# Optimization experiments

Hardware: AMD Instinct MI355X
Metric: run time of the kernel (lower is better)

## Reference

```python
import jax, jax.numpy as jnp
import numpy as np

D_MODEL = 1024
NUM_HEADS = 16
D_K = D_MODEL // NUM_HEADS
THETA = 10000.0
MAX_SEQ_LEN = 2048


def _rope_tables(token_positions):
    # theta^(-2i/d_k) for i in [0, d_k/2)
    inv_freq = THETA ** (-jnp.arange(0, D_K, 2, dtype=jnp.float32) / D_K)
    m_theta = token_positions.astype(jnp.float32)[:, None] * inv_freq[None, :]  # (S, d_k/2)
    return jnp.cos(m_theta), jnp.sin(m_theta)


def _apply_rope(x, cos, sin):
    # x: (B, H, S, d_k); interleaved even/odd pairing
    x1 = x[..., 0::2]
    x2 = x[..., 1::2]
    c = cos[None, None, :, :]
    s = sin[None, None, :, :]
    r1 = x1 * c - x2 * s
    r2 = x1 * s + x2 * c
    return jnp.stack((r1, r2), axis=-1).reshape(x.shape)


def setup_inputs() -> dict:
    key = jax.random.key(0)
    k_x, k_q, k_k, k_v, k_o = jax.random.split(key, 5)
    B, S = 2, 2048
    std = 0.02
    return {
        "x": jax.random.normal(k_x, (B, S, D_MODEL), dtype=jnp.float32),
        "wq": jax.random.normal(k_q, (D_MODEL, D_MODEL), dtype=jnp.float32) * std,
        "wk": jax.random.normal(k_k, (D_MODEL, D_MODEL), dtype=jnp.float32) * std,
        "wv": jax.random.normal(k_v, (D_MODEL, D_MODEL), dtype=jnp.float32) * std,
        "wo": jax.random.normal(k_o, (D_MODEL, D_MODEL), dtype=jnp.float32) * std,
        "token_positions": jnp.arange(S, dtype=jnp.int32),
    }


def reference(x, wq, wk, wv, wo, token_positions):
    B, S, _ = x.shape
    cos, sin = _rope_tables(token_positions)

    # Projections: weight stored as (out, in), applied as x @ W^T
    q = (x @ wq.T).reshape(B, S, NUM_HEADS, D_K).transpose(0, 2, 1, 3)
    k = (x @ wk.T).reshape(B, S, NUM_HEADS, D_K).transpose(0, 2, 1, 3)
    v = (x @ wv.T).reshape(B, S, NUM_HEADS, D_K).transpose(0, 2, 1, 3)

    q = _apply_rope(q, cos, sin)
    k = _apply_rope(k, cos, sin)

    scale = 1.0 / jnp.sqrt(jnp.float32(D_K))
    scores = jnp.einsum("bhqd,bhkd->bhqk", q, k) * scale  # (B, H, S, S)
    causal = jnp.tril(jnp.ones((S, S), dtype=bool))
    scores = jnp.where(causal[None, None, :, :], scores, jnp.finfo(scores.dtype).min)
    probs = jax.nn.softmax(scores, axis=-1)

    out = jnp.einsum("bhqk,bhkd->bhqd", probs, v)  # (B, H, S, d_k)
    out = out.transpose(0, 2, 1, 3).reshape(B, S, D_MODEL)
    return out @ wo.T
```

## Files before the change

kernel.cpp:

```cpp
#include <hip/hip_runtime.h>
#include <hip/hip_bf16.h>
#include <stdint.h>

typedef __attribute__((ext_vector_type(4))) float f32x4;
typedef __attribute__((ext_vector_type(16))) float f32x16;
typedef __bf16 bf16x8v __attribute__((ext_vector_type(8)));
typedef __attribute__((ext_vector_type(4))) unsigned int u32x4;
typedef __attribute__((ext_vector_type(2))) unsigned int u32x2;

constexpr int NB = 2;
constexpr int NS = 2048;
constexpr int ND = 1024;
constexpr int NH = 16;
constexpr int NDK = 64;

__device__ __forceinline__ void gload16(const void* g, void* l) {
    __builtin_amdgcn_global_load_lds(
        (const __attribute__((address_space(1))) unsigned int*)g,
        (__attribute__((address_space(3))) unsigned int*)l, 16, 0, 0);
}

__device__ __forceinline__ unsigned pack_bf16x2(float lo, float hi) {
    unsigned short a = __builtin_bit_cast(unsigned short, (__bf16)lo);
    unsigned short b = __builtin_bit_cast(unsigned short, (__bf16)hi);
    return (unsigned)a | ((unsigned)b << 16);
}

__device__ __forceinline__ float xhalf(float v, int h) {
    const unsigned u = __builtin_bit_cast(unsigned, v);
    const u32x2 r = __builtin_amdgcn_permlane32_swap(u, u, false, false);
    return __builtin_bit_cast(float, h ? r[0] : r[1]);
}

__global__ void __launch_bounds__(256)
prep_kernel(const float* __restrict__ x, const float* __restrict__ wq,
            const float* __restrict__ wk, const float* __restrict__ wv,
            const float* __restrict__ wo, const int* __restrict__ pos,
            __bf16* __restrict__ xb, __bf16* __restrict__ wqb,
            __bf16* __restrict__ wkb, __bf16* __restrict__ wvb,
            __bf16* __restrict__ wob,
            float* __restrict__ cos_t, float* __restrict__ sin_t)
{
    int b = blockIdx.x;
    if (b >= 4096) {
        const int idx = (b - 4096) * 256 + threadIdx.x;
        const int s = idx >> 5, p = idx & 31;
        const float freq = __expf((float)p * (-0.28782313662425572f));
        const float ang = (float)pos[s] * freq;
        float sn, cs;
        sincosf(ang, &sn, &cs);
        cos_t[idx] = cs;
        sin_t[idx] = sn;
        return;
    }
    const float* s; __bf16* d;
    if (b < 2048)      { s = x;  d = xb;            }
    else if (b < 2560) { s = wq; d = wqb; b -= 2048; }
    else if (b < 3072) { s = wk; d = wkb; b -= 2560; }
    else if (b < 3584) { s = wv; d = wvb; b -= 3072; }
    else               { s = wo; d = wob; b -= 3584; }
    const size_t i = ((size_t)b * 256 + threadIdx.x) * 8;
    const f32x4 v0 = *(const f32x4*)(s + i);
    const f32x4 v1 = *(const f32x4*)(s + i + 4);
    bf16x8v o;
#pragma unroll
    for (int j = 0; j < 4; ++j) { o[j] = (__bf16)v0[j]; o[4+j] = (__bf16)v1[j]; }
    *(bf16x8v*)(d + i) = o;
}

__device__ __forceinline__ void epi_one(
    f32x4 a, int fm, int fn, int bm, int wm, int g, int c, int mode, int h_out,
    const float* __restrict__ cos_t, const float* __restrict__ sin_t,
    __bf16* __restrict__ qw, __bf16* __restrict__ kw, __bf16* __restrict__ vtw)
{
    const int m0 = bm * 128 + wm * 64 + fm * 16 + g * 4;
    const int bI = m0 >> 11, s0 = m0 & (NS - 1);
    const int d = fn * 16 + c;
    float v0 = a[0], v1 = a[1], v2 = a[2], v3 = a[3];
    if (mode < 2) {
        const int p = d >> 1;
        const bool odd = (d & 1);
        const float sc = (mode == 0) ? 0.18033688011112042f : 1.0f;
#define ROPE1(V, I)                                                        \
        {                                                                  \
            const float cs = cos_t[(s0 + (I)) * 32 + p];                   \
            const float sn = sin_t[(s0 + (I)) * 32 + p];                   \
            const float oth = __shfl_xor(V, 1, 64);                       \
            V = (odd ? (oth * sn + V * cs) : (V * cs - oth * sn)) * sc;    \
        }
        ROPE1(v0, 0) ROPE1(v1, 1) ROPE1(v2, 2) ROPE1(v3, 3)
#undef ROPE1
        __bf16* dq = (mode == 0) ? qw : kw;
        __bf16* b = dq + (((size_t)bI * NH + h_out) * NS + s0) * NDK + d;
        b[0] = (__bf16)v0; b[NDK] = (__bf16)v1;
        b[2 * NDK] = (__bf16)v2; b[3 * NDK] = (__bf16)v3;
    } else {
        ushort4 pk;
        pk.x = __builtin_bit_cast(unsigned short, (__bf16)v0);
        pk.y = __builtin_bit_cast(unsigned short, (__bf16)v1);
        pk.z = __builtin_bit_cast(unsigned short, (__bf16)v2);
        pk.w = __builtin_bit_cast(unsigned short, (__bf16)v3);
        *(ushort4*)&vtw[(((size_t)bI * NH + h_out) * NDK + d) * NS + s0] = pk;
    }
}

__global__ void __launch_bounds__(256, 3)
qkv_kernel(const __bf16* __restrict__ xb,
           const __bf16* __restrict__ wqb, const __bf16* __restrict__ wkb,
           const __bf16* __restrict__ wvb,
           const float* __restrict__ cos_t, const float* __restrict__ sin_t,
           __bf16* __restrict__ qw, __bf16* __restrict__ kw,
           __bf16* __restrict__ vtw)
{
    __shared__ __align__(16) __bf16 a_lds[128 * 64];
    __shared__ __align__(16) __bf16 b_lds[128 * 64];

    const int t = threadIdx.x, w = t >> 6, lane = t & 63;
    const int g = lane >> 4, c = lane & 15;
    const int bm = blockIdx.x, bn = blockIdx.y;
    const int mode = bn >> 3, nblk = bn & 7;
    const __bf16* wsel = (mode == 0) ? wqb : (mode == 1) ? wkb : wvb;
    const int wm = w >> 1, wn = w & 1;

    f32x4 acc00 = {}, acc01 = {}, acc02 = {}, acc03 = {};
    f32x4 acc10 = {}, acc11 = {}, acc12 = {}, acc13 = {};
    f32x4 acc20 = {}, acc21 = {}, acc22 = {}, acc23 = {};
    f32x4 acc30 = {}, acc31 = {}, acc32 = {}, acc33 = {};

    const int csw = ((t & 7) ^ ((t >> 3) & 7)) * 8;
    const int sx = c & 7;
    const int sl0 = (g ^ sx) * 8;
    const int sl1 = ((4 + g) ^ sx) * 8;
    const __bf16* arow = &a_lds[(wm * 64 + c) * 64];
    const __bf16* brow = &b_lds[(wn * 64 + c) * 64];

    for (int kt = 0; kt < 16; ++kt) {
        __syncthreads();
#pragma unroll
        for (int j = 0; j < 4; ++j) {
            const int r = (j * 256 + t) >> 3;
            gload16(xb   + (size_t)(bm   * 128 + r) * ND + kt * 64 + csw,
                    &a_lds[j * 2048 + w * 512]);
            gload16(wsel + (size_t)(nblk * 128 + r) * ND + kt * 64 + csw,
                    &b_lds[j * 2048 + w * 512]);
        }
        __syncthreads();
#define MM(FM, FN, AF, BF) acc##FM##FN = __builtin_amdgcn_mfma_f32_16x16x32_bf16( \
        AF, BF, acc##FM##FN, 0, 0, 0);
#define KKSTEP(SL)                                                            \
        {                                                                     \
            const bf16x8v af0 = *(const bf16x8v*)(arow + (SL));               \
            const bf16x8v af1 = *(const bf16x8v*)(arow + 1024 + (SL));        \
            const bf16x8v af2 = *(const bf16x8v*)(arow + 2048 + (SL));        \
            const bf16x8v af3 = *(const bf16x8v*)(arow + 3072 + (SL));        \
            const bf16x8v bf0 = *(const bf16x8v*)(brow + (SL));               \
            const bf16x8v bf1 = *(const bf16x8v*)(brow + 1024 + (SL));        \
            const bf16x8v bf2 = *(const bf16x8v*)(brow + 2048 + (SL));        \
            const bf16x8v bf3 = *(const bf16x8v*)(brow + 3072 + (SL));        \
            MM(0,0,af0,bf0) MM(0,1,af0,bf1) MM(0,2,af0,bf2) MM(0,3,af0,bf3)   \
            MM(1,0,af1,bf0) MM(1,1,af1,bf1) MM(1,2,af1,bf2) MM(1,3,af1,bf3)   \
            MM(2,0,af2,bf0) MM(2,1,af2,bf1) MM(2,2,af2,bf2) MM(2,3,af2,bf3)   \
            MM(3,0,af3,bf0) MM(3,1,af3,bf1) MM(3,2,af3,bf2) MM(3,3,af3,bf3)   \
        }
        KKSTEP(sl0)
        KKSTEP(sl1)
#undef KKSTEP
#undef MM
    }

    const int h_out = nblk * 2 + wn;
#define EP(FM, FN) epi_one(acc##FM##FN, FM, FN, bm, wm, g, c, mode, h_out, \
                           cos_t, sin_t, qw, kw, vtw);
    EP(0,0) EP(0,1) EP(0,2) EP(0,3)
    EP(1,0) EP(1,1) EP(1,2) EP(1,3)
    EP(2,0) EP(2,1) EP(2,2) EP(2,3)
    EP(3,0) EP(3,1) EP(3,2) EP(3,3)
#undef EP
}

__global__ void __launch_bounds__(512)
__attribute__((amdgpu_waves_per_eu(4, 4)))
attn_kernel(const __bf16* __restrict__ q, const __bf16* __restrict__ k,
            const __bf16* __restrict__ vt, __bf16* __restrict__ o)
{
    __shared__ __align__(16) __bf16 smem[33280];

    const int t = threadIdx.x, w = t >> 6, lane = t & 63;
    const int c = lane & 31, h = lane >> 5;
    const int qs = w >> 1, half = w & 1;
    const int bid = blockIdx.x;
    const int idx = bid >> 5;
    const int qt16 = (idx < 8) ? (15 - idx) : (idx - 8);
    const int bh = bid & 31;
    const size_t base = (size_t)bh * NS * NDK;
    const int q0 = qt16 * 128 + qs * 32;
    const int kd_w = 2 * qt16 + (qs >> 1);
    const int NH0 = qt16 + 1;
    const int Tof = half * NH0;

    bf16x8v qf0, qf1, qf2, qf3;
    {
        const __bf16* qp = q + base + (size_t)(q0 + c) * NDK + h * 8;
        qf0 = *(const bf16x8v*)(qp);
        qf1 = *(const bf16x8v*)(qp + 16);
        qf2 = *(const bf16x8v*)(qp + 32);
        qf3 = *(const bf16x8v*)(qp + 48);
    }

    const int r0 = t >> 3, cb0 = t & 7;
    const int csw = (cb0 ^ (r0 & 7)) * 8;
    const __bf16* ksrc = k  + base + (size_t)r0 * NDK + csw;
    const __bf16* vsrc = vt + base + (size_t)r0 * NS  + csw;

    const int rbase = (c >> 3) * 520 + (c & 7) * 64;
    const int sl0 = ((0 + h) ^ (c & 7)) * 8;
    const int sl1 = ((2 + h) ^ (c & 7)) * 8;
    const int sl2 = ((4 + h) ^ (c & 7)) * 8;
    const int sl3 = ((6 + h) ^ (c & 7)) * 8;

#define STAGE(I) {                                                             \
        gload16(ksrc + (size_t)(I) * 4096,                                     \
                smem + ((I) & 1) * 4160 + w * 520);                            \
        gload16(ksrc + (size_t)((I) + NH0) * 4096,                             \
                smem + 8320 + ((I) & 1) * 4160 + w * 520);                     \
        gload16(vsrc + (I) * 64,                                               \
                smem + 16640 + ((I) & 1) * 4160 + w * 520);                    \
        gload16(vsrc + ((I) + NH0) * 64,                                       \
                smem + 16640 + 8320 + ((I) & 1) * 4160 + w * 520); }

    float mrow = -3e38f, lrow = 0.f;
    f32x16 oa0 = {}, oa1 = {};

#define COMPUTE(T, I) {                                                       \
    const __bf16* kb = smem + half * 8320 + ((I) & 1) * 4160;                 \
    const __bf16* vb = kb + 16640;                                            \
    f32x16 st0 = {}, st1 = {};                                                \
    {                                                                         \
        const __bf16* klo = kb + rbase;                                      \
        const __bf16* khi = kb + rbase + 2080;                               \
        st0 = __builtin_amdgcn_mfma_f32_32x32x16_bf16(                        \
            *(const bf16x8v*)(klo + sl0), qf0, st0, 0, 0, 0);                 \
        st1 = __builtin_amdgcn_mfma_f32_32x32x16_bf16(                        \
            *(const bf16x8v*)(khi + sl0), qf0, st1, 0, 0, 0);                 \
        st0 = __builtin_amdgcn_mfma_f32_32x32x16_bf16(                        \
            *(const bf16x8v*)(klo + sl1), qf1, st0, 0, 0, 0);                 \
        st1 = __builtin_amdgcn_mfma_f32_32x32x16_bf16(                        \
            *(const bf16x8v*)(khi + sl1), qf1, st1, 0, 0, 0);                 \
        st0 = __builtin_amdgcn_mfma_f32_32x32x16_bf16(                        \
            *(const bf16x8v*)(klo + sl2), qf2, st0, 0, 0, 0);                 \
        st1 = __builtin_amdgcn_mfma_f32_32x32x16_bf16(                        \
            *(const bf16x8v*)(khi + sl2), qf2, st1, 0, 0, 0);                 \
        st0 = __builtin_amdgcn_mfma_f32_32x32x16_bf16(                        \
            *(const bf16x8v*)(klo + sl3), qf3, st0, 0, 0, 0);                 \
        st1 = __builtin_amdgcn_mfma_f32_32x32x16_bf16(                        \
            *(const bf16x8v*)(khi + sl3), qf3, st1, 0, 0, 0);                 \
    }                                                                         \
    if ((T) == kd_w) {                                                        \
        const int kb0 = (T) * 64, qg = q0 + c;                                \
        _Pragma("unroll")                                                     \
        for (int r = 0; r < 16; ++r) {                                        \
            const int krow = (r & 3) + 8 * (r >> 2) + 4 * h;                  \
            if (kb0 + krow > qg)      st0[r] = -3e38f;                        \
            if (kb0 + 32 + krow > qg) st1[r] = -3e38f;                        \
        }                                                                     \
    }                                                                         \
    {                                                                         \
        const float p0 = MX3(st0[0], st0[1], st0[2]);                         \
        const float p1 = MX3(st0[3], st0[4], st0[5]);                         \
        const float p2 = MX3(st0[6], st0[7], st0[8]);                         \
        const float p3 = MX3(st0[9], st0[10], st0[11]);                       \
        const float p4 = MX3(st0[12], st0[13], st0[14]);                      \
        const float p5 = MX3(st0[15], st1[0], st1[1]);                        \
        const float p6 = MX3(st1[2], st1[3], st1[4]);                         \
        const float p7 = MX3(st1[5], st1[6], st1[7]);                         \
        const float p8 = MX3(st1[8], st1[9], st1[10]);                        \
        const float p9 = MX3(st1[11], st1[12], st1[13]);                      \
        const float pa = fmaxf(st1[14], st1[15]);                             \
        const float t0_ = MX3(p0, p1, p2);                                    \
        const float t1_ = MX3(p3, p4, p5);                                    \
        const float t2_ = MX3(p6, p7, p8);                                    \
        float mt = MX3(MX3(t0_, t1_, t2_), p9, pa);                           \
        mt = fmaxf(mt, xhalf(mt, h));                                         \
        if (!__all(mt - mrow <= 8.0f)) {                                      \
            const float mn = fmaxf(mrow, mt);                                 \
            const float al = __builtin_amdgcn_exp2f(mrow - mn);               \
            mrow = mn;                                                        \
            lrow *= al;                                                       \
            _Pragma("unroll")                                                 \
            for (int r = 0; r < 16; ++r) { oa0[r] *= al; oa1[r] *= al; }      \
        }                                                                     \
    }                                                                         \
    _Pragma("unroll")                                                         \
    for (int r = 0; r < 16; ++r) st0[r] = __builtin_amdgcn_exp2f(st0[r] - mrow); \
    _Pragma("unroll")                                                         \
    for (int r = 0; r < 16; ++r) st1[r] = __builtin_amdgcn_exp2f(st1[r] - mrow); \
    {                                                                         \
        const float s00 = (st0[0] + st0[1]) + (st0[2] + st0[3]);              \
        const float s01 = (st0[4] + st0[5]) + (st0[6] + st0[7]);              \
        const float s02 = (st0[8] + st0[9]) + (st0[10] + st0[11]);            \
        const float s03 = (st0[12] + st0[13]) + (st0[14] + st0[15]);          \
        const float s10 = (st1[0] + st1[1]) + (st1[2] + st1[3]);              \
        const float s11 = (st1[4] + st1[5]) + (st1[6] + st1[7]);              \
        const float s12 = (st1[8] + st1[9]) + (st1[10] + st1[11]);            \
        const float s13 = (st1[12] + st1[13]) + (st1[14] + st1[15]);          \
        float rs = ((s00 + s01) + (s02 + s03)) + ((s10 + s11) + (s12 + s13)); \
        rs += xhalf(rs, h);                                                   \
        lrow += rs;                                                           \
    }                                                                         \
    PV_STEP(st0, 0, sl0)                                                      \
    PV_STEP(st0, 1, sl1)                                                      \
    PV_STEP(st1, 0, sl2)                                                      \
    PV_STEP(st1, 1, sl3)                                                      \
}

#define MX3(a, b, cc) fmaxf(fmaxf((a), (b)), (cc))
#define PV_STEP(ST, T, SLT)  {                                                \
    const unsigned w0_ = pack_bf16x2(ST[8*(T)+0], ST[8*(T)+1]);               \
    const unsigned w1_ = pack_bf16x2(ST[8*(T)+2], ST[8*(T)+3]);               \
    const unsigned w2_ = pack_bf16x2(ST[8*(T)+4], ST[8*(T)+5]);               \
    const unsigned w3_ = pack_bf16x2(ST[8*(T)+6], ST[8*(T)+7]);               \
    const u32x2 r02 = __builtin_amdgcn_permlane32_swap(w0_, w2_, false, false); \
    const u32x2 r13 = __builtin_amdgcn_permlane32_swap(w1_, w3_, false, false); \
    const u32x4 pu = { r02[0], r13[0], r02[1], r13[1] };                      \
    const bf16x8v pf = __builtin_bit_cast(bf16x8v, pu);                       \
    const bf16x8v v0_ = *(const bf16x8v*)(vb + rbase + (SLT));                \
    const bf16x8v v1_ = *(const bf16x8v*)(vb + rbase + 2080 + (SLT));         \
    oa0 = __builtin_amdgcn_mfma_f32_32x32x16_bf16(v0_, pf, oa0, 0, 0, 0);     \
    oa1 = __builtin_amdgcn_mfma_f32_32x32x16_bf16(v1_, pf, oa1, 0, 0, 0); }

    STAGE(0)
    __syncthreads();

    for (int i = 0; ; ++i) {
        if (i + 1 < NH0) STAGE(i + 1)
        const int T = Tof + i;
        if (T <= kd_w) COMPUTE(T, i)
        if (i + 1 == NH0) break;
        __syncthreads();
    }
#undef COMPUTE
#undef PV_STEP
#undef MX3
#undef STAGE

    __syncthreads();
    float* mbuf = (float*)smem + qs * 2176;
    if (half) {
#pragma unroll
        for (int r = 0; r < 16; ++r) {
            mbuf[64 * r + lane]        = oa0[r];
            mbuf[64 * (16 + r) + lane] = oa1[r];
        }
        mbuf[64 * 32 + lane] = mrow;
        mbuf[64 * 33 + lane] = lrow;
    }
    __syncthreads();
    if (!half) {
        const float m1 = mbuf[64 * 32 + lane];
        const float l1 = mbuf[64 * 33 + lane];
        const float mm = fmaxf(mrow, m1);
        const float a0 = __builtin_amdgcn_exp2f(mrow - mm);
        const float a1 = __builtin_amdgcn_exp2f(m1 - mm);
        lrow = lrow * a0 + l1 * a1;
#pragma unroll
        for (int r = 0; r < 16; ++r) {
            oa0[r] = oa0[r] * a0 + mbuf[64 * r + lane] * a1;
            oa1[r] = oa1[r] * a0 + mbuf[64 * (16 + r) + lane] * a1;
        }
    }
    __syncthreads();

    if (!half) {
        const float inv = 1.f / lrow;
        __bf16* ol = smem + qs * 2304;
#pragma unroll
        for (int r = 0; r < 16; ++r) {
            const int crow = (r & 3) + 8 * (r >> 2) + 4 * h;
            ol[c * 72 + crow]      = (__bf16)(oa0[r] * inv);
            ol[c * 72 + 32 + crow] = (__bf16)(oa1[r] * inv);
        }
        const int bI = bh >> 4, hh = bh & 15;
        const int qr0 = lane >> 3, cb8 = lane & 7;
#pragma unroll
        for (int mm2 = 0; mm2 < 4; ++mm2) {
            const int qr = qr0 + 8 * mm2;
            const bf16x8v vv = *(const bf16x8v*)&ol[qr * 72 + cb8 * 8];
            *(bf16x8v*)(o + ((size_t)(bI * NS + q0 + qr)) * ND + hh * NDK + cb8 * 8) = vv;
        }
    }
}

__global__ void __launch_bounds__(256, 3)
oproj_kernel(const __bf16* __restrict__ a, const __bf16* __restrict__ wob,
             float* __restrict__ out)
{
    __shared__ __align__(16) __bf16 a_lds[128 * 64];
    __shared__ __align__(16) __bf16 b_lds[128 * 64];

    const int t = threadIdx.x, w = t >> 6, lane = t & 63;
    const int g = lane >> 4, c = lane & 15;
    const int bm = blockIdx.x, bn = blockIdx.y;
    const int wm = w >> 1, wn = w & 1;

    f32x4 acc00 = {}, acc01 = {}, acc02 = {}, acc03 = {};
    f32x4 acc10 = {}, acc11 = {}, acc12 = {}, acc13 = {};
    f32x4 acc20 = {}, acc21 = {}, acc22 = {}, acc23 = {};
    f32x4 acc30 = {}, acc31 = {}, acc32 = {}, acc33 = {};

    const int csw = ((t & 7) ^ ((t >> 3) & 7)) * 8;
    const int sx = c & 7;
    const int sl0 = (g ^ sx) * 8;
    const int sl1 = ((4 + g) ^ sx) * 8;
    const __bf16* arow = &a_lds[(wm * 64 + c) * 64];
    const __bf16* brow = &b_lds[(wn * 64 + c) * 64];

    for (int kt = 0; kt < 16; ++kt) {
        __syncthreads();
#pragma unroll
        for (int j = 0; j < 4; ++j) {
            const int r = (j * 256 + t) >> 3;
            gload16(a   + (size_t)(bm * 128 + r) * ND + kt * 64 + csw,
                    &a_lds[j * 2048 + w * 512]);
            gload16(wob + (size_t)(bn * 128 + r) * ND + kt * 64 + csw,
                    &b_lds[j * 2048 + w * 512]);
        }
        __syncthreads();
#define MM(FM, FN, AF, BF) acc##FM##FN = __builtin_amdgcn_mfma_f32_16x16x32_bf16( \
        AF, BF, acc##FM##FN, 0, 0, 0);
#define KKSTEP(SL)                                                            \
        {                                                                     \
            const bf16x8v af0 = *(const bf16x8v*)(arow + (SL));               \
            const bf16x8v af1 = *(const bf16x8v*)(arow + 1024 + (SL));        \
            const bf16x8v af2 = *(const bf16x8v*)(arow + 2048 + (SL));        \
            const bf16x8v af3 = *(const bf16x8v*)(arow + 3072 + (SL));        \
            const bf16x8v bf0 = *(const bf16x8v*)(brow + (SL));               \
            const bf16x8v bf1 = *(const bf16x8v*)(brow + 1024 + (SL));        \
            const bf16x8v bf2 = *(const bf16x8v*)(brow + 2048 + (SL));        \
            const bf16x8v bf3 = *(const bf16x8v*)(brow + 3072 + (SL));        \
            MM(0,0,af0,bf0) MM(0,1,af0,bf1) MM(0,2,af0,bf2) MM(0,3,af0,bf3)   \
            MM(1,0,af1,bf0) MM(1,1,af1,bf1) MM(1,2,af1,bf2) MM(1,3,af1,bf3)   \
            MM(2,0,af2,bf0) MM(2,1,af2,bf1) MM(2,2,af2,bf2) MM(2,3,af2,bf3)   \
            MM(3,0,af3,bf0) MM(3,1,af3,bf1) MM(3,2,af3,bf2) MM(3,3,af3,bf3)   \
        }
        KKSTEP(sl0)
        KKSTEP(sl1)
#undef KKSTEP
#undef MM
    }

#define EPO(FM, FN, A)                                                     \
    {                                                                      \
        const int m0 = bm * 128 + wm * 64 + (FM) * 16 + g * 4;             \
        const int n = bn * 128 + wn * 64 + (FN) * 16 + c;                  \
        out[(size_t)(m0 + 0) * ND + n] = A[0];                             \
        out[(size_t)(m0 + 1) * ND + n] = A[1];                             \
        out[(size_t)(m0 + 2) * ND + n] = A[2];                             \
        out[(size_t)(m0 + 3) * ND + n] = A[3];                             \
    }
    EPO(0,0,acc00) EPO(0,1,acc01) EPO(0,2,acc02) EPO(0,3,acc03)
    EPO(1,0,acc10) EPO(1,1,acc11) EPO(1,2,acc12) EPO(1,3,acc13)
    EPO(2,0,acc20) EPO(2,1,acc21) EPO(2,2,acc22) EPO(2,3,acc23)
    EPO(3,0,acc30) EPO(3,1,acc31) EPO(3,2,acc32) EPO(3,3,acc33)
#undef EPO
}

extern "C" void kernel_launch(void* const* d_in, const int* in_sizes, int n_in,
                              void* d_out, int out_size, void* d_ws, size_t ws_size,
                              hipStream_t stream)
{
    const float* x  = (const float*)d_in[0];
    const float* wq = (const float*)d_in[1];
    const float* wk = (const float*)d_in[2];
    const float* wv = (const float*)d_in[3];
    const float* wo = (const float*)d_in[4];
    const int*  pos = (const int*)d_in[5];
    float* out = (float*)d_out;
    (void)in_sizes; (void)n_in; (void)out_size; (void)ws_size;

    float* cos_t = (float*)d_ws;
    float* sin_t = cos_t + NS * 32;

    const size_t xel = (size_t)NB * NS * ND;
    const size_t wel = (size_t)ND * ND;
    __bf16* xb  = (__bf16*)(sin_t + NS * 32);
    __bf16* wqb = xb  + xel;
    __bf16* wkb = wqb + wel;
    __bf16* wvb = wkb + wel;
    __bf16* wob = wvb + wel;
    __bf16* qw  = wob + wel;
    __bf16* kw  = qw  + xel;
    __bf16* vtw = kw  + xel;
    __bf16* aw  = vtw + xel;

    prep_kernel<<<4352, 256, 0, stream>>>(x, wq, wk, wv, wo, pos,
                                          xb, wqb, wkb, wvb, wob, cos_t, sin_t);

    dim3 qg(32, 24);
    qkv_kernel<<<qg, 256, 0, stream>>>(xb, wqb, wkb, wvb, cos_t, sin_t, qw, kw, vtw);

    attn_kernel<<<512, 512, 0, stream>>>(qw, kw, vtw, aw);

    dim3 og(32, 8);
    oproj_kernel<<<og, 256, 0, stream>>>(aw, wob, out);
}
```

Before: 98.53 us.

## Process two 32-row query tiles per wave in attention to reuse K/V fragments

The attention kernel now has each wave own 64 query rows, held as two 32-row sets with separate softmax state and accumulators, instead of 32 rows. Each K and V fragment read from LDS now feeds two MFMAs, which halves LDS read traffic per MFMA. The block shrinks from 512 to 256 threads, each thread stages twice as many global-to-LDS loads, and the merge and epilogue handle both query sets. The trade-off is roughly double the accumulator and score registers per wave, plus fewer waves per block, which may lower occupancy and latency hiding.

```diff
diff --git a/kernel.cpp b/kernel.cpp
--- a/kernel.cpp
+++ b/kernel.cpp
@@ -178,8 +178,8 @@
 #undef EP
 }
 
-__global__ void __launch_bounds__(512)
-__attribute__((amdgpu_waves_per_eu(4, 4)))
+__global__ void __launch_bounds__(256)
+__attribute__((amdgpu_waves_per_eu(2, 4)))
 attn_kernel(const __bf16* __restrict__ q, const __bf16* __restrict__ k,
             const __bf16* __restrict__ vt, __bf16* __restrict__ o)
 {
@@ -193,24 +193,31 @@
     const int qt16 = (idx < 8) ? (15 - idx) : (idx - 8);
     const int bh = bid & 31;
     const size_t base = (size_t)bh * NS * NDK;
-    const int q0 = qt16 * 128 + qs * 32;
-    const int kd_w = 2 * qt16 + (qs >> 1);
+    const int q0 = qt16 * 128 + qs * 64;
+    const int kd_w = 2 * qt16 + qs;
     const int NH0 = qt16 + 1;
     const int Tof = half * NH0;
 
-    bf16x8v qf0, qf1, qf2, qf3;
+    bf16x8v qfA0, qfA1, qfA2, qfA3, qfB0, qfB1, qfB2, qfB3;
     {
         const __bf16* qp = q + base + (size_t)(q0 + c) * NDK + h * 8;
-        qf0 = *(const bf16x8v*)(qp);
-        qf1 = *(const bf16x8v*)(qp + 16);
-        qf2 = *(const bf16x8v*)(qp + 32);
-        qf3 = *(const bf16x8v*)(qp + 48);
+        qfA0 = *(const bf16x8v*)(qp);
+        qfA1 = *(const bf16x8v*)(qp + 16);
+        qfA2 = *(const bf16x8v*)(qp + 32);
+        qfA3 = *(const bf16x8v*)(qp + 48);
+        const __bf16* qp2 = qp + (size_t)32 * NDK;
+        qfB0 = *(const bf16x8v*)(qp2);
+        qfB1 = *(const bf16x8v*)(qp2 + 16);
+        qfB2 = *(const bf16x8v*)(qp2 + 32);
+        qfB3 = *(const bf16x8v*)(qp2 + 48);
     }
 
     const int r0 = t >> 3, cb0 = t & 7;
     const int csw = (cb0 ^ (r0 & 7)) * 8;
-    const __bf16* ksrc = k  + base + (size_t)r0 * NDK + csw;
-    const __bf16* vsrc = vt + base + (size_t)r0 * NS  + csw;
+    const __bf16* ksrc  = k  + base + (size_t)r0 * NDK + csw;
+    const __bf16* ksrc2 = ksrc + 32 * NDK;
+    const __bf16* vsrc  = vt + base + (size_t)r0 * NS + csw;
+    const __bf16* vsrc2 = vsrc + (size_t)32 * NS;
 
     const int rbase = (c >> 3) * 520 + (c & 7) * 64;
     const int sl0 = ((0 + h) ^ (c & 7)) * 8;
@@ -218,103 +225,82 @@
     const int sl2 = ((4 + h) ^ (c & 7)) * 8;
     const int sl3 = ((6 + h) ^ (c & 7)) * 8;
 
-#define STAGE(I) {                                                             \
-        gload16(ksrc + (size_t)(I) * 4096,                                     \
-                smem + ((I) & 1) * 4160 + w * 520);                            \
-        gload16(ksrc + (size_t)((I) + NH0) * 4096,                             \
-                smem + 8320 + ((I) & 1) * 4160 + w * 520);                     \
-        gload16(vsrc + (I) * 64,                                               \
-                smem + 16640 + ((I) & 1) * 4160 + w * 520);                    \
-        gload16(vsrc + ((I) + NH0) * 64,                                       \
-                smem + 16640 + 8320 + ((I) & 1) * 4160 + w * 520); }
-
-    float mrow = -3e38f, lrow = 0.f;
-    f32x16 oa0 = {}, oa1 = {};
-
-#define COMPUTE(T, I) {                                                       \
-    const __bf16* kb = smem + half * 8320 + ((I) & 1) * 4160;                 \
-    const __bf16* vb = kb + 16640;                                            \
-    f32x16 st0 = {}, st1 = {};                                                \
-    {                                                                         \
-        const __bf16* klo = kb + rbase;                                      \
-        const __bf16* khi = kb + rbase + 2080;                               \
-        st0 = __builtin_amdgcn_mfma_f32_32x32x16_bf16(                        \
-            *(const bf16x8v*)(klo + sl0), qf0, st0, 0, 0, 0);                 \
-        st1 = __builtin_amdgcn_mfma_f32_32x32x16_bf16(                        \
-            *(const bf16x8v*)(khi + sl0), qf0, st1, 0, 0, 0);                 \
-        st0 = __builtin_amdgcn_mfma_f32_32x32x16_bf16(                        \
-            *(const bf16x8v*)(klo + sl1), qf1, st0, 0, 0, 0);                 \
-        st1 = __builtin_amdgcn_mfma_f32_32x32x16_bf16(                        \
-            *(const bf16x8v*)(khi + sl1), qf1, st1, 0, 0, 0);                 \
-        st0 = __builtin_amdgcn_mfma_f32_32x32x16_bf16(                        \
-            *(const bf16x8v*)(klo + sl2), qf2, st0, 0, 0, 0);                 \
-        st1 = __builtin_amdgcn_mfma_f32_32x32x16_bf16(                        \
-            *(const bf16x8v*)(khi + sl2), qf2, st1, 0, 0, 0);                 \
-        st0 = __builtin_amdgcn_mfma_f32_32x32x16_bf16(                        \
-            *(const bf16x8v*)(klo + sl3), qf3, st0, 0, 0, 0);                 \
-        st1 = __builtin_amdgcn_mfma_f32_32x32x16_bf16(                        \
-            *(const bf16x8v*)(khi + sl3), qf3, st1, 0, 0, 0);                 \
-    }                                                                         \
-    if ((T) == kd_w) {                                                        \
-        const int kb0 = (T) * 64, qg = q0 + c;                                \
+#define STAGE(I) {                                                               \
+        gload16(ksrc  + (size_t)(I) * 4096,                                      \
+                smem + ((I) & 1) * 4160 + w * 520);                              \
+        gload16(ksrc2 + (size_t)(I) * 4096,                                      \
+                smem + ((I) & 1) * 4160 + (w + 4) * 520);                        \
+        gload16(ksrc  + (size_t)((I) + NH0) * 4096,                              \
+                smem + 8320 + ((I) & 1) * 4160 + w * 520);                       \
+        gload16(ksrc2 + (size_t)((I) + NH0) * 4096,                              \
+                smem + 8320 + ((I) & 1) * 4160 + (w + 4) * 520);                 \
+        gload16(vsrc  + (I) * 64,                                                \
+                smem + 16640 + ((I) & 1) * 4160 + w * 520);                      \
+        gload16(vsrc2 + (I) * 64,                                                \
+                smem + 16640 + ((I) & 1) * 4160 + (w + 4) * 520);                \
+        gload16(vsrc  + ((I) + NH0) * 64,                                        \
+                smem + 16640 + 8320 + ((I) & 1) * 4160 + w * 520);               \
+        gload16(vsrc2 + ((I) + NH0) * 64,                                        \
+                smem + 16640 + 8320 + ((I) & 1) * 4160 + (w + 4) * 520); }
+
+    float mrowA = -3e38f, lrowA = 0.f, mrowB = -3e38f, lrowB = 0.f;
+    f32x16 oaA0 = {}, oaA1 = {}, oaB0 = {}, oaB1 = {};
+
+#define MX3(a, b, cc) fmaxf(fmaxf((a), (b)), (cc))
+
+#define QKSTEP(SL, QFA, QFB) {                                                \
+    const bf16x8v klo_ = *(const bf16x8v*)(kbr + (SL));                       \
+    const bf16x8v khi_ = *(const bf16x8v*)(kbr + 2080 + (SL));                \
+    stA0 = __builtin_amdgcn_mfma_f32_32x32x16_bf16(klo_, QFA, stA0, 0, 0, 0); \
+    stA1 = __builtin_amdgcn_mfma_f32_32x32x16_bf16(khi_, QFA, stA1, 0, 0, 0); \
+    stB0 = __builtin_amdgcn_mfma_f32_32x32x16_bf16(klo_, QFB, stB0, 0, 0, 0); \
+    stB1 = __builtin_amdgcn_mfma_f32_32x32x16_bf16(khi_, QFB, stB1, 0, 0, 0); }
+
+#define SOFTMAX(ST0, ST1, MROW, LROW, OA0, OA1) {                             \
+    const float p0 = MX3(ST0[0], ST0[1], ST0[2]);                             \
+    const float p1 = MX3(ST0[3], ST0[4], ST0[5]);                             \
+    const float p2 = MX3(ST0[6], ST0[7], ST0[8]);                             \
+    const float p3 = MX3(ST0[9], ST0[10], ST0[11]);                           \
+    const float p4 = MX3(ST0[12], ST0[13], ST0[14]);                          \
+    const float p5 = MX3(ST0[15], ST1[0], ST1[1]);                            \
+    const float p6 = MX3(ST1[2], ST1[3], ST1[4]);                             \
+    const float p7 = MX3(ST1[5], ST1[6], ST1[7]);                             \
+    const float p8 = MX3(ST1[8], ST1[9], ST1[10]);                            \
+    const float p9 = MX3(ST1[11], ST1[12], ST1[13]);                          \
+    const float pa = fmaxf(ST1[14], ST1[15]);                                 \
+    const float t0_ = MX3(p0, p1, p2);                                        \
+    const float t1_ = MX3(p3, p4, p5);                                        \
+    const float t2_ = MX3(p6, p7, p8);                                        \
+    float mt = MX3(MX3(t0_, t1_, t2_), p9, pa);                               \
+    mt = fmaxf(mt, xhalf(mt, h));                                             \
+    if (!__all(mt - MROW <= 8.0f)) {                                          \
+        const float mn = fmaxf(MROW, mt);                                     \
+        const float al = __builtin_amdgcn_exp2f(MROW - mn);                   \
+        MROW = mn;                                                            \
+        LROW *= al;                                                           \
         _Pragma("unroll")                                                     \
-        for (int r = 0; r < 16; ++r) {                                        \
-            const int krow = (r & 3) + 8 * (r >> 2) + 4 * h;                  \
-            if (kb0 + krow > qg)      st0[r] = -3e38f;                        \
-            if (kb0 + 32 + krow > qg) st1[r] = -3e38f;                        \
-        }                                                                     \
-    }                                                                         \
-    {                                                                         \
-        const float p0 = MX3(st0[0], st0[1], st0[2]);                         \
-        const float p1 = MX3(st0[3], st0[4], st0[5]);                         \
-        const float p2 = MX3(st0[6], st0[7], st0[8]);                         \
-        const float p3 = MX3(st0[9], st0[10], st0[11]);                       \
-        const float p4 = MX3(st0[12], st0[13], st0[14]);                      \
-        const float p5 = MX3(st0[15], st1[0], st1[1]);                        \
-        const float p6 = MX3(st1[2], st1[3], st1[4]);                         \
-        const float p7 = MX3(st1[5], st1[6], st1[7]);                         \
-        const float p8 = MX3(st1[8], st1[9], st1[10]);                        \
-        const float p9 = MX3(st1[11], st1[12], st1[13]);                      \
-        const float pa = fmaxf(st1[14], st1[15]);                             \
-        const float t0_ = MX3(p0, p1, p2);                                    \
-        const float t1_ = MX3(p3, p4, p5);                                    \
-        const float t2_ = MX3(p6, p7, p8);                                    \
-        float mt = MX3(MX3(t0_, t1_, t2_), p9, pa);                           \
-        mt = fmaxf(mt, xhalf(mt, h));                                         \
-        if (!__all(mt - mrow <= 8.0f)) {                                      \
-            const float mn = fmaxf(mrow, mt);                                 \
-            const float al = __builtin_amdgcn_exp2f(mrow - mn);               \
-            mrow = mn;                                                        \
-            lrow *= al;                                                       \
-            _Pragma("unroll")                                                 \
-            for (int r = 0; r < 16; ++r) { oa0[r] *= al; oa1[r] *= al; }      \
-        }                                                                     \
+        for (int r = 0; r < 16; ++r) { OA0[r] *= al; OA1[r] *= al; }          \
     }                                                                         \
     _Pragma("unroll")                                                         \
-    for (int r = 0; r < 16; ++r) st0[r] = __builtin_amdgcn_exp2f(st0[r] - mrow); \
+    for (int r = 0; r < 16; ++r) ST0[r] = __builtin_amdgcn_exp2f(ST0[r] - MROW); \
     _Pragma("unroll")                                                         \
-    for (int r = 0; r < 16; ++r) st1[r] = __builtin_amdgcn_exp2f(st1[r] - mrow); \
+    for (int r = 0; r < 16; ++r) ST1[r] = __builtin_amdgcn_exp2f(ST1[r] - MROW); \
     {                                                                         \
-        const float s00 = (st0[0] + st0[1]) + (st0[2] + st0[3]);              \
-        const float s01 = (st0[4] + st0[5]) + (st0[6] + st0[7]);              \
-        const float s02 = (st0[8] + st0[9]) + (st0[10] + st0[11]);            \
-        const float s03 = (st0[12] + st0[13]) + (st0[14] + st0[15]);          \
-        const float s10 = (st1[0] + st1[1]) + (st1[2] + st1[3]);              \
-        const float s11 = (st1[4] + st1[5]) + (st1[6] + st1[7]);              \
-        const float s12 = (st1[8] + st1[9]) + (st1[10] + st1[11]);            \
-        const float s13 = (st1[12] + st1[13]) + (st1[14] + st1[15]);          \
+        const float s00 = (ST0[0] + ST0[1]) + (ST0[2] + ST0[3]);              \
+        const float s01 = (ST0[4] + ST0[5]) + (ST0[6] + ST0[7]);              \
+        const float s02 = (ST0[8] + ST0[9]) + (ST0[10] + ST0[11]);            \
+        const float s03 = (ST0[12] + ST0[13]) + (ST0[14] + ST0[15]);          \
+        const float s10 = (ST1[0] + ST1[1]) + (ST1[2] + ST1[3]);              \
+        const float s11 = (ST1[4] + ST1[5]) + (ST1[6] + ST1[7]);              \
+        const float s12 = (ST1[8] + ST1[9]) + (ST1[10] + ST1[11]);            \
+        const float s13 = (ST1[12] + ST1[13]) + (ST1[14] + ST1[15]);          \
         float rs = ((s00 + s01) + (s02 + s03)) + ((s10 + s11) + (s12 + s13)); \
         rs += xhalf(rs, h);                                                   \
-        lrow += rs;                                                           \
+        LROW += rs;                                                           \
     }                                                                         \
-    PV_STEP(st0, 0, sl0)                                                      \
-    PV_STEP(st0, 1, sl1)                                                      \
-    PV_STEP(st1, 0, sl2)                                                      \
-    PV_STEP(st1, 1, sl3)                                                      \
-}
-
-#define MX3(a, b, cc) fmaxf(fmaxf((a), (b)), (cc))
-#define PV_STEP(ST, T, SLT)  {                                                \
+}
+
+#define PVONE(ST, T, VL, VH, OA0, OA1) {                                      \
     const unsigned w0_ = pack_bf16x2(ST[8*(T)+0], ST[8*(T)+1]);               \
     const unsigned w1_ = pack_bf16x2(ST[8*(T)+2], ST[8*(T)+3]);               \
     const unsigned w2_ = pack_bf16x2(ST[8*(T)+4], ST[8*(T)+5]);               \
@@ -323,10 +309,43 @@
     const u32x2 r13 = __builtin_amdgcn_permlane32_swap(w1_, w3_, false, false); \
     const u32x4 pu = { r02[0], r13[0], r02[1], r13[1] };                      \
     const bf16x8v pf = __builtin_bit_cast(bf16x8v, pu);                       \
-    const bf16x8v v0_ = *(const bf16x8v*)(vb + rbase + (SLT));                \
-    const bf16x8v v1_ = *(const bf16x8v*)(vb + rbase + 2080 + (SLT));         \
-    oa0 = __builtin_amdgcn_mfma_f32_32x32x16_bf16(v0_, pf, oa0, 0, 0, 0);     \
-    oa1 = __builtin_amdgcn_mfma_f32_32x32x16_bf16(v1_, pf, oa1, 0, 0, 0); }
+    OA0 = __builtin_amdgcn_mfma_f32_32x32x16_bf16(VL, pf, OA0, 0, 0, 0);      \
+    OA1 = __builtin_amdgcn_mfma_f32_32x32x16_bf16(VH, pf, OA1, 0, 0, 0); }
+
+#define PVSTEP(SL, STA, STB, T) {                                             \
+    const bf16x8v vl_ = *(const bf16x8v*)(vbr + (SL));                        \
+    const bf16x8v vh_ = *(const bf16x8v*)(vbr + 2080 + (SL));                 \
+    PVONE(STA, T, vl_, vh_, oaA0, oaA1)                                       \
+    PVONE(STB, T, vl_, vh_, oaB0, oaB1) }
+
+#define COMPUTE(T, I) {                                                       \
+    const __bf16* kb = smem + half * 8320 + ((I) & 1) * 4160;                 \
+    const __bf16* kbr = kb + rbase;                                           \
+    const __bf16* vbr = kbr + 16640;                                          \
+    f32x16 stA0 = {}, stA1 = {}, stB0 = {}, stB1 = {};                        \
+    QKSTEP(sl0, qfA0, qfB0)                                                   \
+    QKSTEP(sl1, qfA1, qfB1)                                                   \
+    QKSTEP(sl2, qfA2, qfB2)                                                   \
+    QKSTEP(sl3, qfA3, qfB3)                                                   \
+    if ((T) == kd_w) {                                                        \
+        const int kb0 = (T) * 64;                                             \
+        const int qgA = q0 + c, qgB = q0 + 32 + c;                            \
+        _Pragma("unroll")                                                     \
+        for (int r = 0; r < 16; ++r) {                                        \
+            const int krow = (r & 3) + 8 * (r >> 2) + 4 * h;                  \
+            if (kb0 + krow > qgA)      stA0[r] = -3e38f;                      \
+            if (kb0 + 32 + krow > qgA) stA1[r] = -3e38f;                      \
+            if (kb0 + krow > qgB)      stB0[r] = -3e38f;                      \
+            if (kb0 + 32 + krow > qgB) stB1[r] = -3e38f;                      \
+        }                                                                     \
+    }                                                                         \
+    SOFTMAX(stA0, stA1, mrowA, lrowA, oaA0, oaA1)                             \
+    SOFTMAX(stB0, stB1, mrowB, lrowB, oaB0, oaB1)                             \
+    PVSTEP(sl0, stA0, stB0, 0)                                                \
+    PVSTEP(sl1, stA0, stB0, 1)                                                \
+    PVSTEP(sl2, stA1, stB1, 0)                                                \
+    PVSTEP(sl3, stA1, stB1, 1)                                                \
+}
 
     STAGE(0)
     __syncthreads();
@@ -339,53 +358,92 @@
         __syncthreads();
     }
 #undef COMPUTE
-#undef PV_STEP
+#undef PVSTEP
+#undef PVONE
+#undef SOFTMAX
+#undef QKSTEP
 #undef MX3
 #undef STAGE
 
     __syncthreads();
-    float* mbuf = (float*)smem + qs * 2176;
+    float* mbuf = (float*)smem + qs * 4352;
     if (half) {
 #pragma unroll
         for (int r = 0; r < 16; ++r) {
-            mbuf[64 * r + lane]        = oa0[r];
-            mbuf[64 * (16 + r) + lane] = oa1[r];
-        }
-        mbuf[64 * 32 + lane] = mrow;
-        mbuf[64 * 33 + lane] = lrow;
+            mbuf[64 * r + lane]        = oaA0[r];
+            mbuf[64 * (16 + r) + lane] = oaA1[r];
+            mbuf[64 * (32 + r) + lane] = oaB0[r];
+            mbuf[64 * (48 + r) + lane] = oaB1[r];
+        }
+        mbuf[64 * 64 + lane] = mrowA;
+        mbuf[64 * 65 + lane] = lrowA;
+        mbuf[64 * 66 + lane] = mrowB;
+        mbuf[64 * 67 + lane] = lrowB;
     }
     __syncthreads();
     if (!half) {
-        const float m1 = mbuf[64 * 32 + lane];
-        const float l1 = mbuf[64 * 33 + lane];
-        const float mm = fmaxf(mrow, m1);
-        const float a0 = __builtin_amdgcn_exp2f(mrow - mm);
-        const float a1 = __builtin_amdgcn_exp2f(m1 - mm);
-        lrow = lrow * a0 + l1 * a1;
-#pragma unroll
-        for (int r = 0; r < 16; ++r) {
-            oa0[r] = oa0[r] * a0 + mbuf[64 * r + lane] * a1;
-            oa1[r] = oa1[r] * a0 + mbuf[64 * (16 + r) + lane] * a1;
+        {
+            const float m1 = mbuf[64 * 64 + lane];
+            const float l1 = mbuf[64 * 65 + lane];
+            const float mm = fmaxf(mrowA, m1);
+            const float a0 = __builtin_amdgcn_exp2f(mrowA - mm);
+            const float a1 = __builtin_amdgcn_exp2f(m1 - mm);
+            lrowA = lrowA * a0 + l1 * a1;
+#pragma unroll
+            for (int r = 0; r < 16; ++r) {
+                oaA0[r] = oaA0[r] * a0 + mbuf[64 * r + lane] * a1;
+                oaA1[r] = oaA1[r] * a0 + mbuf[64 * (16 + r) + lane] * a1;
+            }
+        }
+        {
+            const float m1 = mbuf[64 * 66 + lane];
+            const float l1 = mbuf[64 * 67 + lane];
+            const float mm = fmaxf(mrowB, m1);
+            const float a0 = __builtin_amdgcn_exp2f(mrowB - mm);
+            const float a1 = __builtin_amdgcn_exp2f(m1 - mm);
+            lrowB = lrowB * a0 + l1 * a1;
+#pragma unroll
+            for (int r = 0; r < 16; ++r) {
+                oaB0[r] = oaB0[r] * a0 + mbuf[64 * (32 + r) + lane] * a1;
+                oaB1[r] = oaB1[r] * a0 + mbuf[64 * (48 + r) + lane] * a1;
+            }
         }
     }
     __syncthreads();
 
     if (!half) {
-        const float inv = 1.f / lrow;
-        __bf16* ol = smem + qs * 2304;
-#pragma unroll
-        for (int r = 0; r < 16; ++r) {
-            const int crow = (r & 3) + 8 * (r >> 2) + 4 * h;
-            ol[c * 72 + crow]      = (__bf16)(oa0[r] * inv);
-            ol[c * 72 + 32 + crow] = (__bf16)(oa1[r] * inv);
-        }
         const int bI = bh >> 4, hh = bh & 15;
         const int qr0 = lane >> 3, cb8 = lane & 7;
-#pragma unroll
-        for (int mm2 = 0; mm2 < 4; ++mm2) {
-            const int qr = qr0 + 8 * mm2;
-            const bf16x8v vv = *(const bf16x8v*)&ol[qr * 72 + cb8 * 8];
-            *(bf16x8v*)(o + ((size_t)(bI * NS + q0 + qr)) * ND + hh * NDK + cb8 * 8) = vv;
+        __bf16* ol = smem + qs * 2304;
+        {
+            const float inv = 1.f / lrowA;
+#pragma unroll
+            for (int r = 0; r < 16; ++r) {
+                const int crow = (r & 3) + 8 * (r >> 2) + 4 * h;
+                ol[c * 72 + crow]      = (__bf16)(oaA0[r] * inv);
+                ol[c * 72 + 32 + crow] = (__bf16)(oaA1[r] * inv);
+            }
+#pragma unroll
+            for (int mm2 = 0; mm2 < 4; ++mm2) {
+                const int qr = qr0 + 8 * mm2;
+                const bf16x8v vv = *(const bf16x8v*)&ol[qr * 72 + cb8 * 8];
+                *(bf16x8v*)(o + ((size_t)(bI * NS + q0 + qr)) * ND + hh * NDK + cb8 * 8) = vv;
+            }
+        }
+        {
+            const float inv = 1.f / lrowB;
+#pragma unroll
+            for (int r = 0; r < 16; ++r) {
+                const int crow = (r & 3) + 8 * (r >> 2) + 4 * h;
+                ol[c * 72 + crow]      = (__bf16)(oaB0[r] * inv);
+                ol[c * 72 + 32 + crow] = (__bf16)(oaB1[r] * inv);
+            }
+#pragma unroll
+            for (int mm2 = 0; mm2 < 4; ++mm2) {
+                const int qr = qr0 + 8 * mm2;
+                const bf16x8v vv = *(const bf16x8v*)&ol[qr * 72 + cb8 * 8];
+                *(bf16x8v*)(o + ((size_t)(bI * NS + q0 + 32 + qr)) * ND + hh * NDK + cb8 * 8) = vv;
+            }
         }
     }
 }
@@ -498,7 +556,7 @@
     dim3 qg(32, 24);
     qkv_kernel<<<qg, 256, 0, stream>>>(xb, wqb, wkb, wvb, cos_t, sin_t, qw, kw, vtw);
 
-    attn_kernel<<<512, 512, 0, stream>>>(qw, kw, vtw, aw);
+    attn_kernel<<<512, 256, 0, stream>>>(qw, kw, vtw, aw);
 
     dim3 og(32, 8);
     oproj_kernel<<<og, 256, 0, stream>>>(aw, wob, out);
```

Result: slower. 101.0 us (+2.6%).
